# Kernel tuning notes

Hardware: AMD Instinct MI355X
Metric: run time of the kernel (lower is better)

## Reference

```python
import jax, jax.numpy as jnp
import numpy as np

NU = 1.0  # degrees of freedom of the Student-t / Tsallis softmax


def setup_inputs() -> dict:
    key = jax.random.key(0)
    k1, k2, k3, k4 = jax.random.split(key, 4)
    B, Nx, Nh, Ny = 8192, 2048, 512, 1024
    x = jax.random.normal(k1, (B, Nx), dtype=jnp.float32)
    W_fc = jax.random.normal(k2, (Nh, Nx), dtype=jnp.float32) * (1.0 / np.sqrt(Nx))
    b_fc = jax.random.normal(k3, (Nh,), dtype=jnp.float32) * 0.01
    W_q = jax.random.normal(k4, (Ny, Nh), dtype=jnp.float32) * (1.0 / np.sqrt(Nh))
    return {"x": x, "W_fc": W_fc, "b_fc": b_fc, "W_q": W_q}


def reference(x, W_fc, b_fc, W_q):
    # x: [B, Nx] -> relu -> Linear(Nx, Nh) -> relu
    h = jax.nn.relu(jax.nn.relu(x) @ W_fc.T + b_fc)  # [B, Nh]
    # Quadratic layer: squared Euclidean distance to each class prototype.
    # ||h - w_j||^2 = ||h||^2 - 2 h.w_j + ||w_j||^2  (avoids [B, Ny, Nh] tensor)
    d = (jnp.sum(h * h, axis=-1, keepdims=True)
         - 2.0 * (h @ W_q.T)
         + jnp.sum(W_q * W_q, axis=-1))  # [B, Ny]
    d = jnp.maximum(d, 0.0)  # guard tiny negatives from fp cancellation
    # LogTSoftmax: p_j \propto (1 + d_j/nu)^{-(nu+1)/2}
    t = (-(NU + 1.0) / 2.0) * jnp.log1p(d / NU)  # [B, Ny]
    return t - jax.scipy.special.logsumexp(t, axis=-1, keepdims=True)
```

## Files before the change

kernel.cpp:

```cpp
#include <hip/hip_runtime.h>
#include <stdint.h>
#include <stddef.h>

#define B_ROWS 8192
#define NX 2048
#define NH 512
#define NY 1024

#define X_ELEMS (B_ROWS * NX)
#define EW_ELEMS (X_ELEMS + NH * NX)
#define EW_BLOCKS (EW_ELEMS / (8 * 256))
#define WQ_BLOCKS (NY / 4)

typedef __attribute__((ext_vector_type(8))) short bf16x8;
typedef __attribute__((ext_vector_type(4))) float f32x4;

static __device__ __forceinline__ unsigned short f2bf(float f) {
    union { float f; unsigned int u; } c; c.f = f;
    unsigned int r = 0x7FFFu + ((c.u >> 16) & 1u);
    return (unsigned short)((c.u + r) >> 16);
}

static __device__ __forceinline__ void glld16(const void* g, void* l) {
    __builtin_amdgcn_global_load_lds(
        (const __attribute__((address_space(1))) unsigned int*)g,
        (__attribute__((address_space(3))) unsigned int*)l, 16, 0, 0);
}

__global__ __launch_bounds__(256) void prep_kernel(const float* __restrict__ x,
                                                   const float* __restrict__ wfc,
                                                   const float* __restrict__ wq,
                                                   unsigned short* __restrict__ xb,
                                                   unsigned short* __restrict__ wfcb,
                                                   unsigned short* __restrict__ wqb,
                                                   float* __restrict__ wqsq,
                                                   float* __restrict__ hsq) {
    const int bid = blockIdx.x;
    const int tid = threadIdx.x;
    if (bid < EW_BLOCKS) {
        size_t idx = ((size_t)bid * 256 + tid) * 8;
        if (idx < (size_t)X_ELEMS) {
            float4 a = *(const float4*)&x[idx];
            float4 b = *(const float4*)&x[idx + 4];
            bf16x8 o;
            o[0] = (short)f2bf(fmaxf(a.x, 0.f)); o[1] = (short)f2bf(fmaxf(a.y, 0.f));
            o[2] = (short)f2bf(fmaxf(a.z, 0.f)); o[3] = (short)f2bf(fmaxf(a.w, 0.f));
            o[4] = (short)f2bf(fmaxf(b.x, 0.f)); o[5] = (short)f2bf(fmaxf(b.y, 0.f));
            o[6] = (short)f2bf(fmaxf(b.z, 0.f)); o[7] = (short)f2bf(fmaxf(b.w, 0.f));
            *(bf16x8*)&xb[idx] = o;
        } else {
            size_t off = idx - X_ELEMS;
            float4 a = *(const float4*)&wfc[off];
            float4 b = *(const float4*)&wfc[off + 4];
            bf16x8 o;
            o[0] = (short)f2bf(a.x); o[1] = (short)f2bf(a.y);
            o[2] = (short)f2bf(a.z); o[3] = (short)f2bf(a.w);
            o[4] = (short)f2bf(b.x); o[5] = (short)f2bf(b.y);
            o[6] = (short)f2bf(b.z); o[7] = (short)f2bf(b.w);
            *(bf16x8*)&wfcb[off] = o;
        }
    } else {
        const int b2 = bid - EW_BLOCKS;
        const int lane = tid & 63;
        const int row = b2 * 4 + (tid >> 6);
        const float* p = wq + (size_t)row * NH + lane * 8;
        float4 a = *(const float4*)p;
        float4 b = *(const float4*)(p + 4);
        bf16x8 o;
        o[0] = (short)f2bf(a.x); o[1] = (short)f2bf(a.y);
        o[2] = (short)f2bf(a.z); o[3] = (short)f2bf(a.w);
        o[4] = (short)f2bf(b.x); o[5] = (short)f2bf(b.y);
        o[6] = (short)f2bf(b.z); o[7] = (short)f2bf(b.w);
        *(bf16x8*)&wqb[(size_t)row * NH + lane * 8] = o;
        float s = a.x*a.x + a.y*a.y + a.z*a.z + a.w*a.w
                + b.x*b.x + b.y*b.y + b.z*b.z + b.w*b.w;
        #pragma unroll
        for (int off = 32; off > 0; off >>= 1) s += __shfl_xor(s, off);
        if (lane == 0) wqsq[row] = s;
        if (tid < 32) hsq[b2 * 32 + tid] = 0.0f;
    }
}

__global__ __launch_bounds__(512, 4) void gemm1_kernel(const unsigned short* __restrict__ xb,
                                                       const unsigned short* __restrict__ wfcb,
                                                       const float* __restrict__ b_fc,
                                                       unsigned short* __restrict__ hb,
                                                       float* __restrict__ hsq) {
    __shared__ unsigned char smem[24576];
    unsigned char* AsB = smem;
    unsigned char* BsB = smem + 16384;

    const int tid = threadIdx.x;
    const int lane = tid & 63;
    const int wave = tid >> 6;
    const int wm = wave & 3;
    const int wn = wave >> 2;
    const int quad = lane >> 4;
    const int r = lane & 15;

    const int bid = blockIdx.x;
    const int c_ = bid & 7, q_ = bid >> 3;
    const int n0 = (q_ & 7) * 64;
    const int m0 = ((c_ << 3) | (q_ >> 3)) * 128;

    f32x4 acc[2][2];
    #pragma unroll
    for (int i = 0; i < 2; ++i)
        #pragma unroll
        for (int j = 0; j < 2; ++j) acc[i][j] = (f32x4)(0.0f);

    const int lrow = lane >> 2;
    const int gch = (lane & 3) ^ ((lrow >> 1) & 3);
    const int fsw = (quad ^ ((r >> 1) & 3)) * 16;

    const char* asrc = (const char*)xb + (size_t)(m0 + wave * 16 + lrow) * (NX * 2) + gch * 16;
    const char* bsrc = (const char*)wfcb + (size_t)(n0 + (wave & 3) * 16 + lrow) * (NX * 2) + gch * 16;

    auto stage = [&](int buf, int k0) {
        glld16(asrc + (size_t)k0 * 2, AsB + buf * 8192 + wave * 1024);
        if (wave < 4)
            glld16(bsrc + (size_t)k0 * 2, BsB + buf * 4096 + wave * 1024);
    };

    stage(0, 0);
    #pragma unroll 1
    for (int it = 0; it < NX / 32; ++it) {
        __syncthreads();
        if (it + 1 < NX / 32) stage((it + 1) & 1, it * 32 + 32);
        const unsigned char* ab = AsB + (it & 1) * 8192;
        const unsigned char* bb = BsB + (it & 1) * 4096;
        bf16x8 af[2], bfv[2];
        #pragma unroll
        for (int i = 0; i < 2; ++i)
            af[i] = *(const bf16x8*)(ab + (wm * 32 + i * 16 + r) * 64 + fsw);
        #pragma unroll
        for (int j = 0; j < 2; ++j)
            bfv[j] = *(const bf16x8*)(bb + (wn * 32 + j * 16 + r) * 64 + fsw);
        #pragma unroll
        for (int i = 0; i < 2; ++i)
            #pragma unroll
            for (int j = 0; j < 2; ++j)
                acc[i][j] = __builtin_amdgcn_mfma_f32_16x16x32_bf16(af[i], bfv[j], acc[i][j], 0, 0, 0);
    }

    float p[2][4];
    #pragma unroll
    for (int i = 0; i < 2; ++i)
        #pragma unroll
        for (int rr = 0; rr < 4; ++rr) p[i][rr] = 0.0f;

    #pragma unroll
    for (int j = 0; j < 2; ++j) {
        int col = n0 + wn * 32 + j * 16 + r;
        float bias = b_fc[col];
        #pragma unroll
        for (int i = 0; i < 2; ++i) {
            int rowb = m0 + wm * 32 + i * 16 + quad * 4;
            #pragma unroll
            for (int rr = 0; rr < 4; ++rr) {
                float v = fmaxf(acc[i][j][rr] + bias, 0.0f);
                hb[(size_t)(rowb + rr) * NH + col] = f2bf(v);
                p[i][rr] += v * v;
            }
        }
    }
    #pragma unroll
    for (int mask = 1; mask < 16; mask <<= 1)
        #pragma unroll
        for (int i = 0; i < 2; ++i)
            #pragma unroll
            for (int rr = 0; rr < 4; ++rr)
                p[i][rr] += __shfl_xor(p[i][rr], mask);
    if (r == 0) {
        #pragma unroll
        for (int i = 0; i < 2; ++i)
            #pragma unroll
            for (int rr = 0; rr < 4; ++rr)
                atomicAdd(&hsq[m0 + wm * 32 + i * 16 + quad * 4 + rr], p[i][rr]);
    }
}

__global__ __launch_bounds__(512, 4) void gemm2_kernel(const unsigned short* __restrict__ hb,
                                                       const unsigned short* __restrict__ wqb,
                                                       const float* __restrict__ hsq,
                                                       const float* __restrict__ wqsq,
                                                       float* __restrict__ out) {
    __shared__ unsigned char smem[67584];
    char* BsB = (char*)smem;
    char* AsB = (char*)smem + 65536;

    const int tid = threadIdx.x;
    const int lane = tid & 63;
    const int wave = tid >> 6;
    const int quad = lane >> 4;
    const int r = lane & 15;
    const int m0 = blockIdx.x * 32;

    f32x4 acc[2][8];
    #pragma unroll
    for (int i = 0; i < 2; ++i)
        #pragma unroll
        for (int j = 0; j < 8; ++j) acc[i][j] = (f32x4)(0.0f);

    const int lrow = lane >> 2;
    const int gch = (lane & 3) ^ ((lrow >> 1) & 3);
    const int fsw = (quad ^ ((r >> 1) & 3)) * 16;

    const char* bsrc = (const char*)wqb + (size_t)(wave * 128 + lrow) * (NH * 2) + gch * 16;
    const char* asrc = (const char*)hb + (size_t)(m0 + wave * 16 + lrow) * (NH * 2) + gch * 16;

    auto stage = [&](int k0) {
        #pragma unroll
        for (int c = 0; c < 8; ++c)
            glld16(bsrc + (size_t)(c * 16 * NH + k0) * 2,
                   BsB + (wave * 128 + c * 16) * 64);
        if (wave < 2)
            glld16(asrc + (size_t)k0 * 2, AsB + wave * 1024);
    };

    #pragma unroll 1
    for (int it = 0; it < NH / 32; ++it) {
        stage(it * 32);
        __syncthreads();
        bf16x8 af[2];
        #pragma unroll
        for (int i = 0; i < 2; ++i)
            af[i] = *(const bf16x8*)(AsB + (i * 16 + r) * 64 + fsw);
        #pragma unroll
        for (int jh = 0; jh < 2; ++jh) {
            bf16x8 bfv[4];
            #pragma unroll
            for (int j = 0; j < 4; ++j)
                bfv[j] = *(const bf16x8*)(BsB + (wave * 128 + jh * 64 + j * 16 + r) * 64 + fsw);
            #pragma unroll
            for (int i = 0; i < 2; ++i)
                #pragma unroll
                for (int j = 0; j < 4; ++j)
                    acc[i][jh * 4 + j] = __builtin_amdgcn_mfma_f32_16x16x32_bf16(af[i], bfv[j], acc[i][jh * 4 + j], 0, 0, 0);
        }
        __syncthreads();
    }

    float hs_[2][4];
    #pragma unroll
    for (int i = 0; i < 2; ++i)
        #pragma unroll
        for (int rr = 0; rr < 4; ++rr)
            hs_[i][rr] = hsq[m0 + i * 16 + quad * 4 + rr];

    float srow[2][4];
    #pragma unroll
    for (int i = 0; i < 2; ++i)
        #pragma unroll
        for (int rr = 0; rr < 4; ++rr) srow[i][rr] = 0.0f;

    #pragma unroll
    for (int j = 0; j < 8; ++j) {
        float wqv = wqsq[wave * 128 + j * 16 + r];
        #pragma unroll
        for (int i = 0; i < 2; ++i) {
            #pragma unroll
            for (int rr = 0; rr < 4; ++rr) {
                float d = hs_[i][rr] - 2.0f * acc[i][j][rr] + wqv;
                d = fmaxf(d, 0.0f);
                float onepd = 1.0f + d;
                srow[i][rr] += __builtin_amdgcn_rcpf(onepd);
                acc[i][j][rr] = -__logf(onepd);
            }
        }
    }
    #pragma unroll
    for (int mask = 1; mask < 16; mask <<= 1)
        #pragma unroll
        for (int i = 0; i < 2; ++i)
            #pragma unroll
            for (int rr = 0; rr < 4; ++rr)
                srow[i][rr] += __shfl_xor(srow[i][rr], mask);

    float* smemF = (float*)smem;
    __syncthreads();
    if (r == 0) {
        #pragma unroll
        for (int i = 0; i < 2; ++i)
            #pragma unroll
            for (int rr = 0; rr < 4; ++rr)
                smemF[wave * 32 + i * 16 + quad * 4 + rr] = srow[i][rr];
    }
    __syncthreads();
    if (tid < 32) {
        float S = 0.0f;
        #pragma unroll
        for (int w = 0; w < 8; ++w) S += smemF[w * 32 + tid];
        smemF[256 + tid] = __logf(S);
    }
    __syncthreads();

    #pragma unroll
    for (int i = 0; i < 2; ++i) {
        #pragma unroll
        for (int rr = 0; rr < 4; ++rr) {
            float l = smemF[256 + i * 16 + quad * 4 + rr];
            size_t rowoff = (size_t)(m0 + i * 16 + quad * 4 + rr) * NY + wave * 128 + r;
            #pragma unroll
            for (int j = 0; j < 8; ++j)
                out[rowoff + j * 16] = acc[i][j][rr] - l;
        }
    }
}

extern "C" void kernel_launch(void* const* d_in, const int* in_sizes, int n_in,
                              void* d_out, int out_size, void* d_ws, size_t ws_size,
                              hipStream_t stream) {
    const float* x    = (const float*)d_in[0];
    const float* W_fc = (const float*)d_in[1];
    const float* b_fc = (const float*)d_in[2];
    const float* W_q  = (const float*)d_in[3];
    float* out = (float*)d_out;

    char* ws = (char*)d_ws;
    unsigned short* xb   = (unsigned short*)(ws);
    unsigned short* wfcb = (unsigned short*)(ws + 33554432);
    unsigned short* wqb  = (unsigned short*)(ws + 35651584);
    float*          wqsq = (float*)(ws + 36700160);
    unsigned short* hb   = (unsigned short*)(ws + 36704256);
    float*          hsq  = (float*)(ws + 45092864);

    prep_kernel<<<EW_BLOCKS + WQ_BLOCKS, 256, 0, stream>>>(x, W_fc, W_q, xb, wfcb, wqb, wqsq, hsq);
    gemm1_kernel<<<512, 512, 0, stream>>>(xb, wfcb, b_fc, hb, hsq);
    gemm2_kernel<<<B_ROWS / 32, 512, 0, stream>>>(hb, wqb, hsq, wqsq, out);
}
```

Before: 177.7 us.

## Double-buffer gemm2 W_q tiles, preload full h tile, and hand-schedule barriers

In gemm2, the whole 32-row h tile is now loaded into LDS once up front, and the W_q slabs are double-buffered so the next K slice loads while the current one feeds MFMAs. LDS grows to 160 KB and launch bounds drop to 2 blocks per CU. In both GEMMs, __syncthreads is replaced with explicit vmcnt waits plus s_barrier and sched_barrier fences, so each loop iteration has a single barrier and prefetches overlap compute. The cost is lower occupancy in gemm2, and the code now depends on the compiler honoring the manual scheduling fences.

```diff
diff --git a/kernel.cpp b/kernel.cpp
--- a/kernel.cpp
+++ b/kernel.cpp
@@ -123,10 +123,14 @@
     };
 
     stage(0, 0);
+    asm volatile("s_waitcnt vmcnt(0)" ::: "memory");
+    __builtin_amdgcn_s_barrier();
+    __builtin_amdgcn_sched_barrier(0);
+
     #pragma unroll 1
     for (int it = 0; it < NX / 32; ++it) {
-        __syncthreads();
         if (it + 1 < NX / 32) stage((it + 1) & 1, it * 32 + 32);
+        __builtin_amdgcn_sched_barrier(0);
         const unsigned char* ab = AsB + (it & 1) * 8192;
         const unsigned char* bb = BsB + (it & 1) * 4096;
         bf16x8 af[2], bfv[2];
@@ -141,6 +145,10 @@
             #pragma unroll
             for (int j = 0; j < 2; ++j)
                 acc[i][j] = __builtin_amdgcn_mfma_f32_16x16x32_bf16(af[i], bfv[j], acc[i][j], 0, 0, 0);
+        __builtin_amdgcn_sched_barrier(0);
+        asm volatile("s_waitcnt vmcnt(0)" ::: "memory");
+        __builtin_amdgcn_s_barrier();
+        __builtin_amdgcn_sched_barrier(0);
     }
 
     float p[2][4];
@@ -180,14 +188,14 @@
     }
 }
 
-__global__ __launch_bounds__(512, 4) void gemm2_kernel(const unsigned short* __restrict__ hb,
+__global__ __launch_bounds__(512, 2) void gemm2_kernel(const unsigned short* __restrict__ hb,
                                                        const unsigned short* __restrict__ wqb,
                                                        const float* __restrict__ hsq,
                                                        const float* __restrict__ wqsq,
                                                        float* __restrict__ out) {
-    __shared__ unsigned char smem[67584];
-    char* BsB = (char*)smem;
-    char* AsB = (char*)smem + 65536;
+    __shared__ unsigned char smem[163840];
+    char* As = (char*)smem;
+    char* Bs = (char*)smem + 32768;
 
     const int tid = threadIdx.x;
     const int lane = tid & 63;
@@ -207,38 +215,52 @@
     const int fsw = (quad ^ ((r >> 1) & 3)) * 16;
 
     const char* bsrc = (const char*)wqb + (size_t)(wave * 128 + lrow) * (NH * 2) + gch * 16;
-    const char* asrc = (const char*)hb + (size_t)(m0 + wave * 16 + lrow) * (NH * 2) + gch * 16;
-
-    auto stage = [&](int k0) {
+
+    auto stageB = [&](int buf, int k0) {
         #pragma unroll
         for (int c = 0; c < 8; ++c)
             glld16(bsrc + (size_t)(c * 16 * NH + k0) * 2,
-                   BsB + (wave * 128 + c * 16) * 64);
-        if (wave < 2)
-            glld16(asrc + (size_t)k0 * 2, AsB + wave * 1024);
+                   Bs + buf * 65536 + (wave * 128 + c * 16) * 64);
     };
+
+    #pragma unroll
+    for (int g = 0; g < 4; ++g) {
+        int slab = 2 * wave + (g >> 1);
+        int half = g & 1;
+        glld16((const char*)hb + (size_t)(m0 + half * 16 + lrow) * (NH * 2) + slab * 64 + gch * 16,
+               As + slab * 2048 + half * 1024);
+    }
+    stageB(0, 0);
+    asm volatile("s_waitcnt vmcnt(0)" ::: "memory");
+    __builtin_amdgcn_s_barrier();
+    __builtin_amdgcn_sched_barrier(0);
 
     #pragma unroll 1
     for (int it = 0; it < NH / 32; ++it) {
-        stage(it * 32);
-        __syncthreads();
+        if (it + 1 < NH / 32) stageB((it + 1) & 1, it * 32 + 32);
+        __builtin_amdgcn_sched_barrier(0);
+        const char* ab = As + it * 2048;
+        const char* bb = Bs + (it & 1) * 65536;
         bf16x8 af[2];
         #pragma unroll
         for (int i = 0; i < 2; ++i)
-            af[i] = *(const bf16x8*)(AsB + (i * 16 + r) * 64 + fsw);
+            af[i] = *(const bf16x8*)(ab + (i * 16 + r) * 64 + fsw);
         #pragma unroll
         for (int jh = 0; jh < 2; ++jh) {
             bf16x8 bfv[4];
             #pragma unroll
             for (int j = 0; j < 4; ++j)
-                bfv[j] = *(const bf16x8*)(BsB + (wave * 128 + jh * 64 + j * 16 + r) * 64 + fsw);
+                bfv[j] = *(const bf16x8*)(bb + (wave * 128 + jh * 64 + j * 16 + r) * 64 + fsw);
             #pragma unroll
             for (int i = 0; i < 2; ++i)
                 #pragma unroll
                 for (int j = 0; j < 4; ++j)
                     acc[i][jh * 4 + j] = __builtin_amdgcn_mfma_f32_16x16x32_bf16(af[i], bfv[j], acc[i][jh * 4 + j], 0, 0, 0);
         }
-        __syncthreads();
+        __builtin_amdgcn_sched_barrier(0);
+        asm volatile("s_waitcnt vmcnt(0)" ::: "memory");
+        __builtin_amdgcn_s_barrier();
+        __builtin_amdgcn_sched_barrier(0);
     }
 
     float hs_[2][4];
@@ -278,7 +300,6 @@
                 srow[i][rr] += __shfl_xor(srow[i][rr], mask);
 
     float* smemF = (float*)smem;
-    __syncthreads();
     if (r == 0) {
         #pragma unroll
         for (int i = 0; i < 2; ++i)
```

Result: no change. 174.3 us (-1.9%).
